# Kernel tuning notes

Hardware: AMD Instinct MI355X
Metric: run time of the kernel (lower is better)

The kernel has to match this reference:

```python
import jax, jax.numpy as jnp
import numpy as np

F = 16384   # n_features
D = 768     # d_model
B = 2       # batch
S = 256     # seq len
C = 16      # connections per downstream feature
M = F * C   # total connections


def setup_inputs() -> dict:
    key = jax.random.key(0)
    k1, k2, k3, k4 = jax.random.split(key, 4)
    up_facts = jax.random.normal(k1, (B, S, F), dtype=jnp.float32)
    down_encoder = jax.random.normal(k2, (F, D), dtype=jnp.float32) * 0.02
    up_decoder = jax.random.normal(k3, (D, F), dtype=jnp.float32) * 0.02
    # connection_mask.nonzero() is row-major: i sorted, C targets per row
    i_indices = jnp.repeat(jnp.arange(F, dtype=jnp.int32), C)  # [M]
    j_indices = jax.random.randint(k4, (M,), 0, F, dtype=jnp.int32)  # [M]
    return {
        "up_facts": up_facts,
        "down_encoder": down_encoder,
        "up_decoder": up_decoder,
        "i_indices": i_indices,
        "j_indices": j_indices,
    }


def reference(up_facts, down_encoder, up_decoder, i_indices, j_indices):
    # up_facts: [B,S,F]; down_encoder: [F,D]; up_decoder: [D,F]
    b, s, f = up_facts.shape
    m = i_indices.shape[0]
    # per-connection virtual weight: values[m] = down_encoder[i[m]] . up_decoder[:, j[m]]
    values = jnp.einsum("md,dm->m", down_encoder[i_indices], up_decoder[:, j_indices])  # [M]
    # gather upstream feature activations and scale
    scaled = up_facts[:, :, j_indices] * values[None, None, :]  # [B,S,M]
    # scatter_add over last axis into downstream feature bins (i is constant across B,S)
    flat = scaled.reshape(b * s, m).T  # [M, B*S]
    contrib = jax.ops.segment_sum(flat, i_indices, num_segments=f)  # [F, B*S]
    return contrib.T.reshape(b, s, f)
```

## Files before the change

### kernel.cpp

```cpp
#include <hip/hip_runtime.h>
#include <hip/hip_bf16.h>

#define F_ 16384
#define D_ 768
#define C_ 16
#define BS_ 512
#define M_ (F_*C_)

static __device__ __forceinline__ float bf2f(unsigned short u) {
    return __uint_as_float(((unsigned int)u) << 16);
}
static __device__ __forceinline__ unsigned short f2bf(float f) {
    return __bfloat16_as_ushort(__float2bfloat16(f));
}

__global__ __launch_bounds__(256) void k_transpose_bf16(const float* __restrict__ in,
                                                        unsigned short* __restrict__ out) {
    __shared__ float tile[64][65];
    int c4 = threadIdx.x & 15;
    int r  = threadIdx.x >> 4;
    int fbase = blockIdx.x * 64;
    int dbase = blockIdx.y * 64;
#pragma unroll
    for (int k = 0; k < 4; ++k) {
        int drow = r + k * 16;
        float4 v = *(const float4*)(in + (size_t)(dbase + drow) * F_ + fbase + c4 * 4);
        tile[drow][c4 * 4 + 0] = v.x;
        tile[drow][c4 * 4 + 1] = v.y;
        tile[drow][c4 * 4 + 2] = v.z;
        tile[drow][c4 * 4 + 3] = v.w;
    }
    __syncthreads();
    int dp = threadIdx.x & 15;
    int fr = threadIdx.x >> 4;
#pragma unroll
    for (int k = 0; k < 4; ++k) {
        int frow = fr + k * 16;
        float v0 = tile[4 * dp + 0][frow];
        float v1 = tile[4 * dp + 1][frow];
        float v2 = tile[4 * dp + 2][frow];
        float v3 = tile[4 * dp + 3][frow];
        uint2 p;
        p.x = ((unsigned int)f2bf(v1) << 16) | (unsigned int)f2bf(v0);
        p.y = ((unsigned int)f2bf(v3) << 16) | (unsigned int)f2bf(v2);
        *(uint2*)(out + (size_t)(fbase + frow) * D_ + dbase + dp * 4) = p;
    }
}

__global__ __launch_bounds__(256) void k_values(const float* __restrict__ enc,
                                                const unsigned short* __restrict__ decT,
                                                const int* __restrict__ jidx,
                                                unsigned int* __restrict__ packed) {
    int f = blockIdx.x;
    int lane = threadIdx.x & 63;
    int wave = threadIdx.x >> 6;
    const float4* erow = (const float4*)(enc + (size_t)f * D_);
    float4 e[3];
    e[0] = erow[lane];
    e[1] = erow[lane + 64];
    e[2] = erow[lane + 128];
    int4 j4 = *(const int4*)(jidx + (f << 4) + (wave << 2));
    int js[4] = {j4.x, j4.y, j4.z, j4.w};
    ushort4 g[4][3];
#pragma unroll
    for (int t = 0; t < 4; ++t) {
        const ushort4* drow = (const ushort4*)(decT + (size_t)js[t] * D_);
        g[t][0] = drow[lane];
        g[t][1] = drow[lane + 64];
        g[t][2] = drow[lane + 128];
    }
#pragma unroll
    for (int t = 0; t < 4; ++t) {
        float acc = 0.f;
#pragma unroll
        for (int k = 0; k < 3; ++k) {
            float4 ev = e[k];
            ushort4 dv = g[t][k];
            acc += ev.x * bf2f(dv.x) + ev.y * bf2f(dv.y)
                 + ev.z * bf2f(dv.z) + ev.w * bf2f(dv.w);
        }
#pragma unroll
        for (int off = 32; off > 0; off >>= 1)
            acc += __shfl_down(acc, off, 64);
        if (lane == 0)
            packed[(f << 4) + (wave << 2) + t] =
                ((unsigned int)f2bf(acc) << 16) | (unsigned int)js[t];
    }
}

__global__ __launch_bounds__(512) void k_out(const float* __restrict__ up,
                                             const unsigned int* __restrict__ packed,
                                             float* __restrict__ out) {
    __shared__ unsigned int rowp[F_];
    int bs0  = (blockIdx.x >> 1) << 1;
    int half = blockIdx.x & 1;
    const float4* u0 = (const float4*)(up + (size_t)bs0 * F_);
    const float4* u1 = (const float4*)(up + (size_t)(bs0 + 1) * F_);
#pragma unroll
    for (int k = 0; k < 8; ++k) {
        int idx = threadIdx.x + k * 512;
        float4 a = u0[idx];
        float4 b = u1[idx];
        uint4 p;
        p.x = ((unsigned int)f2bf(b.x) << 16) | (unsigned int)f2bf(a.x);
        p.y = ((unsigned int)f2bf(b.y) << 16) | (unsigned int)f2bf(a.y);
        p.z = ((unsigned int)f2bf(b.z) << 16) | (unsigned int)f2bf(a.z);
        p.w = ((unsigned int)f2bf(b.w) << 16) | (unsigned int)f2bf(a.w);
        ((uint4*)rowp)[idx] = p;
    }
    __syncthreads();
    int f0 = half << 13;
#pragma unroll 4
    for (int it = 0; it < 16; ++it) {
        int f = f0 + threadIdx.x + it * 512;
        const uint4* sp = (const uint4*)(packed + ((size_t)f << 4));
        float a0 = 0.f, a1 = 0.f;
#pragma unroll
        for (int q = 0; q < 4; ++q) {
            uint4 w = sp[q];
#define CONN(ww) { unsigned int p_ = rowp[(ww) & 0xffffu];                  \
                   float v_ = __uint_as_float((ww) & 0xffff0000u);          \
                   a0 += __uint_as_float(p_ << 16) * v_;                    \
                   a1 += __uint_as_float(p_ & 0xffff0000u) * v_; }
            CONN(w.x) CONN(w.y) CONN(w.z) CONN(w.w)
#undef CONN
        }
        out[(size_t)bs0 * F_ + f] = a0;
        out[(size_t)(bs0 + 1) * F_ + f] = a1;
    }
}

extern "C" void kernel_launch(void* const* d_in, const int* in_sizes, int n_in,
                              void* d_out, int out_size, void* d_ws, size_t ws_size,
                              hipStream_t stream) {
    const float* up   = (const float*)d_in[0];
    const float* enc  = (const float*)d_in[1];
    const float* dec  = (const float*)d_in[2];
    const int*   jidx = (const int*)d_in[4];
    float*       out  = (float*)d_out;

    size_t decT_bytes = (size_t)F_ * D_ * sizeof(unsigned short);
    unsigned short* decT   = (unsigned short*)d_ws;
    unsigned int*   packed = (unsigned int*)((char*)d_ws + decT_bytes);

    k_transpose_bf16<<<dim3(F_ / 64, D_ / 64), 256, 0, stream>>>(dec, decT);
    k_values<<<F_, 256, 0, stream>>>(enc, decT, jidx, packed);
    k_out<<<BS_, 512, 0, stream>>>(up, packed, out);
}
```

Measured before the change: 222.9 us.

## Split value dot-products into d-chunks so gathered decoder rows fit cache

The transposed bf16 decoder is stored as 8 chunks of 96 dims, so each chunk of the gather table (about 3 MB) can stay cache-resident while values are computed chunk by chunk. The encoder tile is staged in shared memory, and the next gather is software-prefetched. Partial dot products are written per chunk, and a new pack kernel sums them and packs them with j. This replaces random 1.5 KB row gathers over a 24 MB table with cache-friendly ones. In exchange it adds a 8×M float partial buffer (8 MB write plus read) and an extra launch.

```diff
diff --git a/kernel.cpp b/kernel.cpp
--- a/kernel.cpp
+++ b/kernel.cpp
@@ -6,6 +6,8 @@
 #define C_ 16
 #define BS_ 512
 #define M_ (F_*C_)
+#define NCHUNK 8
+#define CDIM 96
 
 static __device__ __forceinline__ float bf2f(unsigned short u) {
     return __uint_as_float(((unsigned int)u) << 16);
@@ -14,8 +16,8 @@
     return __bfloat16_as_ushort(__float2bfloat16(f));
 }
 
-__global__ __launch_bounds__(256) void k_transpose_bf16(const float* __restrict__ in,
-                                                        unsigned short* __restrict__ out) {
+__global__ __launch_bounds__(256) void k_transpose_chunked(const float* __restrict__ in,
+                                                           unsigned short* __restrict__ decC) {
     __shared__ float tile[64][65];
     int c4 = threadIdx.x & 15;
     int r  = threadIdx.x >> 4;
@@ -43,49 +45,89 @@
         uint2 p;
         p.x = ((unsigned int)f2bf(v1) << 16) | (unsigned int)f2bf(v0);
         p.y = ((unsigned int)f2bf(v3) << 16) | (unsigned int)f2bf(v2);
-        *(uint2*)(out + (size_t)(fbase + frow) * D_ + dbase + dp * 4) = p;
+        int d  = dbase + dp * 4;
+        int c  = d / CDIM;
+        int dl = d - c * CDIM;
+        *(uint2*)(decC + ((size_t)c * F_ + (fbase + frow)) * CDIM + dl) = p;
     }
 }
 
-__global__ __launch_bounds__(256) void k_values(const float* __restrict__ enc,
-                                                const unsigned short* __restrict__ decT,
-                                                const int* __restrict__ jidx,
-                                                unsigned int* __restrict__ packed) {
-    int f = blockIdx.x;
+__global__ __launch_bounds__(256) void k_values_chunked(const float* __restrict__ enc,
+                                                        const unsigned short* __restrict__ decC,
+                                                        const int* __restrict__ jidx,
+                                                        float* __restrict__ partial) {
+    __shared__ float encS[64 * CDIM];
+    int chunk = blockIdx.x & 7;
+    int mblk  = blockIdx.x >> 3;
+    int m0 = mblk * 1024;
+    int f0 = mblk * 64;
+
+    {
+        float4* s4 = (float4*)encS;
+        const float* eb = enc + (size_t)f0 * D_ + chunk * CDIM;
+#pragma unroll
+        for (int k = 0; k < 6; ++k) {
+            int idx = threadIdx.x + k * 256;
+            int row = idx / 24;
+            int col = idx - row * 24;
+            s4[row * 24 + col] = *(const float4*)(eb + (size_t)row * D_ + col * 4);
+        }
+    }
+    __syncthreads();
+
     int lane = threadIdx.x & 63;
     int wave = threadIdx.x >> 6;
-    const float4* erow = (const float4*)(enc + (size_t)f * D_);
-    float4 e[3];
-    e[0] = erow[lane];
-    e[1] = erow[lane + 64];
-    e[2] = erow[lane + 128];
-    int4 j4 = *(const int4*)(jidx + (f << 4) + (wave << 2));
-    int js[4] = {j4.x, j4.y, j4.z, j4.w};
-    ushort4 g[4][3];
+    int sub  = lane & 7;
+    int cg   = lane >> 3;
+    const unsigned short* dbase_p = decC + (size_t)chunk * F_ * CDIM;
+    const float4* e4 = (const float4*)encS;
+
+    int mmA = (wave << 3) + cg;
+    int jA = jidx[m0 + mmA];
+    const unsigned short* drA = dbase_p + (size_t)jA * CDIM + sub * 12;
+    ushort4 g0 = *(const ushort4*)(drA);
+    ushort4 g1 = *(const ushort4*)(drA + 4);
+    ushort4 g2 = *(const ushort4*)(drA + 8);
+    int jB = jidx[m0 + ((1 * 4 + wave) << 3) + cg];
+
+#pragma unroll 4
+    for (int i = 0; i < 32; ++i) {
+        ushort4 n0, n1, n2;
+        if (i + 1 < 32) {
+            const unsigned short* drN = dbase_p + (size_t)jB * CDIM + sub * 12;
+            n0 = *(const ushort4*)(drN);
+            n1 = *(const ushort4*)(drN + 4);
+            n2 = *(const ushort4*)(drN + 8);
+        }
+        if (i + 2 < 32)
+            jB = jidx[m0 + (((i + 2) * 4 + wave) << 3) + cg];
+
+        int mm = ((i * 4 + wave) << 3) + cg;
+        int fl = mm >> 4;
+        const float4* ep = e4 + fl * 24 + sub * 3;
+        float4 ea = ep[0], eb = ep[1], ec = ep[2];
+        float acc;
+        acc  = ea.x * bf2f(g0.x) + ea.y * bf2f(g0.y) + ea.z * bf2f(g0.z) + ea.w * bf2f(g0.w);
+        acc += eb.x * bf2f(g1.x) + eb.y * bf2f(g1.y) + eb.z * bf2f(g1.z) + eb.w * bf2f(g1.w);
+        acc += ec.x * bf2f(g2.x) + ec.y * bf2f(g2.y) + ec.z * bf2f(g2.z) + ec.w * bf2f(g2.w);
+        acc += __shfl_xor(acc, 1, 64);
+        acc += __shfl_xor(acc, 2, 64);
+        acc += __shfl_xor(acc, 4, 64);
+        if (sub == 0)
+            partial[(size_t)chunk * M_ + m0 + mm] = acc;
+        g0 = n0; g1 = n1; g2 = n2;
+    }
+}
+
+__global__ __launch_bounds__(256) void k_pack(const float* __restrict__ partial,
+                                              const int* __restrict__ jidx,
+                                              unsigned int* __restrict__ packed) {
+    int m = blockIdx.x * 256 + threadIdx.x;
+    float s = 0.f;
 #pragma unroll
-    for (int t = 0; t < 4; ++t) {
-        const ushort4* drow = (const ushort4*)(decT + (size_t)js[t] * D_);
-        g[t][0] = drow[lane];
-        g[t][1] = drow[lane + 64];
-        g[t][2] = drow[lane + 128];
-    }
-#pragma unroll
-    for (int t = 0; t < 4; ++t) {
-        float acc = 0.f;
-#pragma unroll
-        for (int k = 0; k < 3; ++k) {
-            float4 ev = e[k];
-            ushort4 dv = g[t][k];
-            acc += ev.x * bf2f(dv.x) + ev.y * bf2f(dv.y)
-                 + ev.z * bf2f(dv.z) + ev.w * bf2f(dv.w);
-        }
-#pragma unroll
-        for (int off = 32; off > 0; off >>= 1)
-            acc += __shfl_down(acc, off, 64);
-        if (lane == 0)
-            packed[(f << 4) + (wave << 2) + t] =
-                ((unsigned int)f2bf(acc) << 16) | (unsigned int)js[t];
-    }
+    for (int c = 0; c < NCHUNK; ++c)
+        s += partial[(size_t)c * M_ + m];
+    packed[m] = ((unsigned int)f2bf(s) << 16) | (unsigned int)jidx[m];
 }
 
 __global__ __launch_bounds__(512) void k_out(const float* __restrict__ up,
@@ -139,11 +181,14 @@
     const int*   jidx = (const int*)d_in[4];
     float*       out  = (float*)d_out;
 
-    size_t decT_bytes = (size_t)F_ * D_ * sizeof(unsigned short);
-    unsigned short* decT   = (unsigned short*)d_ws;
-    unsigned int*   packed = (unsigned int*)((char*)d_ws + decT_bytes);
+    size_t decC_bytes    = (size_t)NCHUNK * F_ * CDIM * sizeof(unsigned short);
+    size_t partial_bytes = (size_t)NCHUNK * M_ * sizeof(float);
+    unsigned short* decC    = (unsigned short*)d_ws;
+    float*          partial = (float*)((char*)d_ws + decC_bytes);
+    unsigned int*   packed  = (unsigned int*)((char*)d_ws + decC_bytes + partial_bytes);
 
-    k_transpose_bf16<<<dim3(F_ / 64, D_ / 64), 256, 0, stream>>>(dec, decT);
-    k_values<<<F_, 256, 0, stream>>>(enc, decT, jidx, packed);
+    k_transpose_chunked<<<dim3(F_ / 64, D_ / 64), 256, 0, stream>>>(dec, decC);
+    k_values_chunked<<<NCHUNK * (M_ / 1024), 256, 0, stream>>>(enc, decC, jidx, partial);
+    k_pack<<<M_ / 256, 256, 0, stream>>>(partial, jidx, packed);
     k_out<<<BS_, 512, 0, stream>>>(up, packed, out);
 }
```

Result: no change. 223.2 us (+0.1%).
